# Optimization experiments

Hardware: AMD Instinct MI355X
Metric: run time of the kernel (lower is better)

## Reference

```python
import jax, jax.numpy as jnp
import numpy as np

B, N, DIM = 2, 8192, 3
K = 16            # num_neighbours (dilation=1)
R = 2048          # num_representitives
CIN, CL, COUT = 64, 16, 128
K2 = K * K


def _bn(x, g, b):
    # BatchNorm in eval mode with running_mean=0, running_var=1 -> affine
    return x * g + b


def setup_inputs() -> dict:
    key = jax.random.key(0)
    ks = jax.random.split(key, 24)
    r = lambda i, shape, s=1.0: jax.random.normal(ks[i], shape, jnp.float32) * s
    return {
        "points": r(0, (B, N, DIM)),
        "features": r(1, (B, N, CIN)),
        "lift_w": r(2, (CL, DIM), 0.3), "lift_b": r(3, (CL,), 0.1),
        "bn_lift_g": 1.0 + r(4, (CL,), 0.1), "bn_lift_b": r(5, (CL,), 0.1),
        "t1_w": r(6, (K2, DIM * K), 0.1), "t1_b": r(7, (K2,), 0.1),
        "bn1_g": 1.0 + r(8, (K2,), 0.1), "bn1_b": r(9, (K2,), 0.1),
        "t2_w": r(10, (K2, K2), 0.05), "t2_b": r(11, (K2,), 0.1),
        "bn2_g": 1.0 + r(12, (K2,), 0.1), "bn2_b": r(13, (K2,), 0.1),
        "t3_w": r(14, (K2, K2), 0.05), "t3_b": r(15, (K2,), 0.1),
        "bn3_g": 1.0 + r(16, (K2,), 0.1), "bn3_b": r(17, (K2,), 0.1),
        "conv_w": r(18, (COUT, CIN + CL, K), 0.05), "conv_b": r(19, (COUT,), 0.1),
        "rep_idx": jax.random.permutation(ks[20], N)[:R],
    }


def reference(points, features, lift_w, lift_b, bn_lift_g, bn_lift_b,
              t1_w, t1_b, bn1_g, bn1_b, t2_w, t2_b, bn2_g, bn2_b,
              t3_w, t3_b, bn3_g, bn3_b, conv_w, conv_b, rep_idx):
    b, n, _ = points.shape
    # ---- KNN (squared distance is order-equivalent to torch.cdist) ----
    sq = jnp.sum(points * points, -1)                                   # (b,n)
    d2 = sq[:, :, None] + sq[:, None, :] - 2.0 * jnp.einsum('bnd,bmd->bnm', points, points)
    _, idx = jax.lax.top_k(-d2, K + 1)                                  # (b,n,K+1)
    nn_idx = idx[:, :, 1:]                                              # drop self
    # ---- representative sampling + neighbor gather ----
    rep_pos = points[:, rep_idx]                                        # (b,R,3)
    nb_idx = nn_idx[:, rep_idx]                                         # (b,R,K)
    gather = jax.vmap(lambda arr, i: arr[i])
    nbr_pos = gather(points, nb_idx)                                    # (b,R,K,3)
    nbr_feat = gather(features, nb_idx)                                 # (b,R,K,CIN)
    # ---- X_conv ----
    p = (nbr_pos - rep_pos[:, :, None, :]).reshape(b * R, K, DIM)       # centered
    lifted = jax.nn.relu(_bn(p @ lift_w.T + lift_b, bn_lift_g, bn_lift_b))  # (bR,K,CL)
    feat = jnp.concatenate([lifted, nbr_feat.reshape(b * R, K, CIN)], -1)   # (bR,K,CL+CIN)
    pf = p.reshape(b * R, K * DIM)
    h = jax.nn.relu(_bn(pf @ t1_w.T + t1_b, bn1_g, bn1_b))
    h = jax.nn.relu(_bn(h @ t2_w.T + t2_b, bn2_g, bn2_b))
    T = _bn(h @ t3_w.T + t3_b, bn3_g, bn3_b).reshape(b * R, K, K)       # learned transform
    Tf = jnp.einsum('bij,bjc->bic', T, feat)                            # bmm, (bR,K,C)
    # Conv1d(C, COUT, kernel=K) over length K -> single output position
    out = jnp.einsum('bkc,ock->bo', Tf, conv_w) + conv_b                # (bR,COUT)
    return rep_pos, out.reshape(b, R, COUT)
```

## Files before the change

kernel.cpp:

```cpp
#include <hip/hip_runtime.h>
#include <float.h>

#define Bn 2
#define Nn 8192
#define Rr 2048
#define Kk 16
#define CIN 64
#define CL 16
#define COUT 128
#define K2c 256
#define GT (Bn*Rr)
#define FD (CL+CIN)
#define KC (Kk*FD)
#define MGB 8
#define SPLITK 4
#define CCAP 128

__global__ __launch_bounds__(256) void prep_kernel(
    const float* __restrict__ t1_w, const float* __restrict__ t2_w,
    const float* __restrict__ t3_w, const float* __restrict__ conv_w,
    const float* __restrict__ points,
    float* __restrict__ t1t, float* __restrict__ t2t,
    float* __restrict__ t3t, float* __restrict__ wp,
    float4* __restrict__ pts4)
{
  int i = blockIdx.x * 256 + threadIdx.x;
  if (i < K2c*48) { int j = i / 48, k = i - j*48; t1t[k*K2c + j] = t1_w[i]; }
  if (i < K2c*K2c) { int j = i >> 8, k = i & 255; t2t[k*K2c + j] = t2_w[i]; t3t[k*K2c + j] = t3_w[i]; }
  if (i < COUT*KC) {
    int o = i / KC, ck = i - o*KC;
    int c = ck >> 4, k = ck & 15;
    wp[(k*FD + c)*COUT + o] = conv_w[i];
  }
  if (i < Bn*Nn) {
    float x = points[i*3+0], y = points[i*3+1], z = points[i*3+2];
    float sq = __fadd_rn(__fadd_rn(__fmul_rn(x,x), __fmul_rn(y,y)), __fmul_rn(z,z));
    pts4[i] = make_float4(x, y, z, sq);
  }
}

__global__ __launch_bounds__(512, 4) void knn_kernel(
    const float4* __restrict__ pts4, const int* __restrict__ rep_idx,
    int* __restrict__ nb_idx, float* __restrict__ p_out,
    float* __restrict__ rep_pos_out)
{
  __shared__ float cbuf[8][512];
  __shared__ unsigned long long coll[8][CCAP];
  __shared__ float Lst[8][64];
  __shared__ float4 qS[8];
  __shared__ float  tauS[8];
  __shared__ int    ccnt[8];

  int t    = threadIdx.x;
  int lane = t & 63;
  int w    = t >> 6;
  int g0   = blockIdx.x * 8;
  int b    = g0 >> 11;
  const float4* pb4 = pts4 + (size_t)b*Nn;

  if (t < 8) {
    int g = g0 + t;
    int r = g & 2047;
    qS[t] = pb4[rep_idx[r]];
    ccnt[t] = 0;
  }
  __syncthreads();

  float qx[8], qy[8], qz[8], qw[8];
  #pragma unroll
  for (int q = 0; q < 8; q++) {
    float4 Q = qS[q];
    qx[q] = __uint_as_float(__builtin_amdgcn_readfirstlane(__float_as_uint(Q.x)));
    qy[q] = __uint_as_float(__builtin_amdgcn_readfirstlane(__float_as_uint(Q.y)));
    qz[q] = __uint_as_float(__builtin_amdgcn_readfirstlane(__float_as_uint(Q.z)));
    qw[q] = __uint_as_float(__builtin_amdgcn_readfirstlane(__float_as_uint(Q.w)));
  }

  float m[8];
  #pragma unroll
  for (int q = 0; q < 8; q++) m[q] = FLT_MAX;
  for (int i0 = 0; i0 < 16; i0 += 4) {
    float4 P0 = pb4[t + 512*(i0+0)];
    float4 P1 = pb4[t + 512*(i0+1)];
    float4 P2 = pb4[t + 512*(i0+2)];
    float4 P3 = pb4[t + 512*(i0+3)];
    #pragma unroll
    for (int q = 0; q < 8; q++) {
      float d0 = __fsub_rn(__fadd_rn(qw[q], P0.w), __fmul_rn(2.0f,
                 __fmaf_rn(qz[q], P0.z, __fmaf_rn(qy[q], P0.y, __fmul_rn(qx[q], P0.x)))));
      float d1 = __fsub_rn(__fadd_rn(qw[q], P1.w), __fmul_rn(2.0f,
                 __fmaf_rn(qz[q], P1.z, __fmaf_rn(qy[q], P1.y, __fmul_rn(qx[q], P1.x)))));
      float d2 = __fsub_rn(__fadd_rn(qw[q], P2.w), __fmul_rn(2.0f,
                 __fmaf_rn(qz[q], P2.z, __fmaf_rn(qy[q], P2.y, __fmul_rn(qx[q], P2.x)))));
      float d3 = __fsub_rn(__fadd_rn(qw[q], P3.w), __fmul_rn(2.0f,
                 __fmaf_rn(qz[q], P3.z, __fmaf_rn(qy[q], P3.y, __fmul_rn(qx[q], P3.x)))));
      m[q] = fminf(fminf(fminf(m[q], d0), fminf(d1, d2)), d3);
    }
  }

  #pragma unroll
  for (int q = 0; q < 8; q++) cbuf[q][t] = m[q];
  __syncthreads();

  {
    float C0 = FLT_MAX, C1 = FLT_MAX, C2 = FLT_MAX;
    #pragma unroll
    for (int j = 0; j < 8; j++) {
      float v = cbuf[w][lane + 64*j];
      float n2 = __builtin_amdgcn_fmed3f(C1, C2, v);
      float n1 = __builtin_amdgcn_fmed3f(C0, C1, v);
      float n0 = fminf(C0, v);
      C0 = n0; C1 = n1; C2 = n2;
    }
    Lst[w][lane] = C2;
  }
  __syncthreads();
  {
    float L = Lst[w][lane];
    int rk = 0;
    #pragma unroll 8
    for (int i = 0; i < 64; i++) {
      float Li = Lst[w][i];
      rk += (Li < L || (Li == L && i < lane)) ? 1 : 0;
    }
    if (rk == 5) tauS[w] = L;
  }
  __syncthreads();

  float tau[8];
  #pragma unroll
  for (int q = 0; q < 8; q++)
    tau[q] = __uint_as_float(__builtin_amdgcn_readfirstlane(__float_as_uint(tauS[q])));

  for (int i0 = 0; i0 < 16; i0 += 4) {
    float4 Pb[4];
    Pb[0] = pb4[t + 512*(i0+0)];
    Pb[1] = pb4[t + 512*(i0+1)];
    Pb[2] = pb4[t + 512*(i0+2)];
    Pb[3] = pb4[t + 512*(i0+3)];
    #pragma unroll
    for (int u = 0; u < 4; u++) {
      float4 P = Pb[u];
      int idx = t + 512*(i0+u);
      #pragma unroll
      for (int q = 0; q < 8; q++) {
        float dot = __fmaf_rn(qz[q], P.z, __fmaf_rn(qy[q], P.y, __fmul_rn(qx[q], P.x)));
        float d2  = __fsub_rn(__fadd_rn(qw[q], P.w), __fmul_rn(2.0f, dot));
        if (d2 <= tau[q]) {
          int pos = atomicAdd(&ccnt[q], 1);
          if (pos < CCAP) {
            unsigned f = __float_as_uint(d2);
            unsigned mono = f ^ ((unsigned)((int)f >> 31) | 0x80000000u);
            coll[q][pos] = ((unsigned long long)mono << 32) | (unsigned)idx;
          }
        }
      }
    }
  }
  __syncthreads();

  int cnt = __builtin_amdgcn_readfirstlane(ccnt[w]);
  if (cnt > CCAP) cnt = CCAP;
  unsigned long long k1 = (lane < cnt)      ? coll[w][lane]      : ~0ull;
  unsigned long long k2 = (lane + 64 < cnt) ? coll[w][lane + 64] : ~0ull;
  int r1 = 0, r2 = 0;
  for (int i = 0; i < cnt; i++) {
    unsigned long long ki = coll[w][i];
    r1 += (ki < k1) ? 1 : 0;
    r2 += (ki < k2) ? 1 : 0;
  }

  int g = g0 + w;
  float4 Q = qS[w];
  if (lane < cnt && r1 >= 1 && r1 <= 16) {
    int om = (int)(k1 & 0xFFFFFFFFull);
    nb_idx[g*Kk + r1 - 1] = om;
    float4 Pm = pb4[om];
    p_out[(g*Kk + r1 - 1)*3 + 0] = __fsub_rn(Pm.x, Q.x);
    p_out[(g*Kk + r1 - 1)*3 + 1] = __fsub_rn(Pm.y, Q.y);
    p_out[(g*Kk + r1 - 1)*3 + 2] = __fsub_rn(Pm.z, Q.z);
  }
  if (lane + 64 < cnt && r2 >= 1 && r2 <= 16) {
    int om = (int)(k2 & 0xFFFFFFFFull);
    nb_idx[g*Kk + r2 - 1] = om;
    float4 Pm = pb4[om];
    p_out[(g*Kk + r2 - 1)*3 + 0] = __fsub_rn(Pm.x, Q.x);
    p_out[(g*Kk + r2 - 1)*3 + 1] = __fsub_rn(Pm.y, Q.y);
    p_out[(g*Kk + r2 - 1)*3 + 2] = __fsub_rn(Pm.z, Q.z);
  }
  if (lane < 3) rep_pos_out[g*3 + lane] = (lane == 0 ? Q.x : (lane == 1 ? Q.y : Q.z));
}

__device__ __forceinline__ void fma_g(float4& a, float hv, const float4& wv) {
  a.x = fmaf(hv, wv.x, a.x);
  a.y = fmaf(hv, wv.y, a.y);
  a.z = fmaf(hv, wv.z, a.z);
  a.w = fmaf(hv, wv.w, a.w);
}

__global__ __launch_bounds__(512) void mlp_kernel(
    const float* __restrict__ p,
    const float* __restrict__ t1t, const float* __restrict__ t1_b,
    const float* __restrict__ g1v, const float* __restrict__ b1v,
    const float* __restrict__ t2t, const float* __restrict__ t2_b,
    const float* __restrict__ g2v, const float* __restrict__ b2v,
    const float* __restrict__ t3t, const float* __restrict__ t3_b,
    const float* __restrict__ g3v, const float* __restrict__ b3v,
    float* __restrict__ T_out)
{
  __shared__ float pf[48][MGB];
  __shared__ float hA[K2c][MGB];
  __shared__ float red[128*66];
  int t = threadIdx.x;
  int w = t >> 6, l = t & 63;
  int g0 = blockIdx.x * MGB;
  for (int e = t; e < MGB*48; e += 512) {
    int g = e / 48, k = e - g*48;
    pf[k][g] = p[(size_t)(g0+g)*48 + k];
  }
  __syncthreads();

  float4 acc[MGB];
  int col = t & 255;
  int h   = t >> 8;
  int cc  = col & 3, lr = col >> 2;

#define LDW(WSRC, K) (*(const float4*)&WSRC[(size_t)(K)*K2c + 4*l])

#define KSTAGE(WSRC, KDIM, HBUF, WB, KK, KNEXT)                        \
  {                                                                    \
    float4 wc = WB;                                                    \
    if ((KNEXT) < KDIM) WB = LDW(WSRC, KNEXT);                         \
    float4 ha = *(const float4*)&HBUF[KK][0];                          \
    float4 hb = *(const float4*)&HBUF[KK][4];                          \
    fma_g(acc[0], ha.x, wc); fma_g(acc[1], ha.y, wc);                  \
    fma_g(acc[2], ha.z, wc); fma_g(acc[3], ha.w, wc);                  \
    fma_g(acc[4], hb.x, wc); fma_g(acc[5], hb.y, wc);                  \
    fma_g(acc[6], hb.z, wc); fma_g(acc[7], hb.w, wc);                  \
  }

#define KLOOP(WSRC, KDIM, HBUF)                                        \
  {                                                                    \
    _Pragma("unroll")                                                  \
    for (int q = 0; q < MGB; q++) acc[q] = make_float4(0.f,0.f,0.f,0.f);\
    float4 wb0 = LDW(WSRC, w);                                         \
    float4 wb1 = (w + 8  < KDIM) ? LDW(WSRC, w + 8)  : wb0;            \
    float4 wb2 = (w + 16 < KDIM) ? LDW(WSRC, w + 16) : wb0;            \
    float4 wb3 = (w + 24 < KDIM) ? LDW(WSRC, w + 24) : wb0;            \
    for (int k = w; k < KDIM; k += 32) {                               \
      KSTAGE(WSRC, KDIM, HBUF, wb0, k,      k + 32)                    \
      if (k + 8  < KDIM) KSTAGE(WSRC, KDIM, HBUF, wb1, k + 8,  k + 40) \
      if (k + 16 < KDIM) KSTAGE(WSRC, KDIM, HBUF, wb2, k + 16, k + 48) \
      if (k + 24 < KDIM) KSTAGE(WSRC, KDIM, HBUF, wb3, k + 24, k + 56) \
    }                                                                  \
  }

#define WRITE_RED()                                                    \
  {                                                                    \
    if (w < 4) {                                                       \
      _Pragma("unroll")                                                \
      for (int q = 0; q < MGB; q++) {                                  \
        red[((w*4 + 0)*8 + q)*66 + l] = acc[q].x;                      \
        red[((w*4 + 1)*8 + q)*66 + l] = acc[q].y;                      \
        red[((w*4 + 2)*8 + q)*66 + l] = acc[q].z;                      \
        red[((w*4 + 3)*8 + q)*66 + l] = acc[q].w;                      \
      }                                                                \
    }                                                                  \
    __syncthreads();                                                   \
    if (w >= 4) {                                                      \
      int w2 = w - 4;                                                  \
      _Pragma("unroll")                                                \
      for (int q = 0; q < MGB; q++) {                                  \
        red[((w2*4 + 0)*8 + q)*66 + l] += acc[q].x;                    \
        red[((w2*4 + 1)*8 + q)*66 + l] += acc[q].y;                    \
        red[((w2*4 + 2)*8 + q)*66 + l] += acc[q].z;                    \
        red[((w2*4 + 3)*8 + q)*66 + l] += acc[q].w;                    \
      }                                                                \
    }                                                                  \
    __syncthreads();                                                   \
  }

#define REDUCE(S)                                                      \
  float S[4] = {0.f, 0.f, 0.f, 0.f};                                   \
  {                                                                    \
    _Pragma("unroll")                                                  \
    for (int ww = 0; ww < 4; ww++) {                                   \
      _Pragma("unroll")                                                \
      for (int qi = 0; qi < 4; qi++)                                   \
        S[qi] += red[((ww*4 + cc)*8 + (h*4 + qi))*66 + lr];            \
    }                                                                  \
  }

  KLOOP(t1t, 48, pf)
  WRITE_RED()
  {
    REDUCE(s)
    float bb = t1_b[col], gg = g1v[col], oo = b1v[col];
    float4 v;
    v.x = fmaxf(fmaf(s[0] + bb, gg, oo), 0.f);
    v.y = fmaxf(fmaf(s[1] + bb, gg, oo), 0.f);
    v.z = fmaxf(fmaf(s[2] + bb, gg, oo), 0.f);
    v.w = fmaxf(fmaf(s[3] + bb, gg, oo), 0.f);
    *(float4*)&hA[col][h*4] = v;
  }
  __syncthreads();

  KLOOP(t2t, K2c, hA)
  WRITE_RED()
  {
    REDUCE(s)
    float bb = t2_b[col], gg = g2v[col], oo = b2v[col];
    float4 v;
    v.x = fmaxf(fmaf(s[0] + bb, gg, oo), 0.f);
    v.y = fmaxf(fmaf(s[1] + bb, gg, oo), 0.f);
    v.z = fmaxf(fmaf(s[2] + bb, gg, oo), 0.f);
    v.w = fmaxf(fmaf(s[3] + bb, gg, oo), 0.f);
    *(float4*)&hA[col][h*4] = v;
  }
  __syncthreads();

  KLOOP(t3t, K2c, hA)
  WRITE_RED()
  {
    REDUCE(s)
    float bb = t3_b[col], gg = g3v[col], oo = b3v[col];
    #pragma unroll
    for (int qi = 0; qi < 4; qi++)
      T_out[(size_t)(g0 + h*4 + qi)*K2c + col] = fmaf(s[qi] + bb, gg, oo);
  }
#undef KLOOP
#undef KSTAGE
#undef LDW
#undef WRITE_RED
#undef REDUCE
}

__global__ __launch_bounds__(256) void tf_kernel(
    const float* __restrict__ T_in, const float* __restrict__ features,
    const float* __restrict__ p, const int* __restrict__ nb_idx,
    const float* __restrict__ lift_w, const float* __restrict__ lift_b,
    const float* __restrict__ bng, const float* __restrict__ bnb,
    float* __restrict__ Tf)
{
  __shared__ float T_s[4*K2c];
  __shared__ float f_s[4*KC];
  __shared__ float ps[4*48];
  __shared__ int   idxs[64];
  __shared__ float lw[48], lb2[16], lg[16], lo[16];
  int t = threadIdx.x;
  int g0 = blockIdx.x * 4;
  int b = g0 / Rr;
  for (int e = t; e < 4*K2c; e += 256) T_s[e] = T_in[(size_t)g0*K2c + e];
  if (t >= 32 && t < 224) {
    int e = t - 32;
    ps[e] = p[(size_t)g0*48 + e];
  }
  if (t < 64) idxs[t] = nb_idx[g0*16 + t];
  if (t >= 64 && t < 112)  lw[t-64]   = lift_w[t-64];
  if (t >= 112 && t < 128) lb2[t-112] = lift_b[t-112];
  if (t >= 224 && t < 240) lg[t-224]  = bng[t-224];
  if (t >= 240)            lo[t-240]  = bnb[t-240];
  __syncthreads();

  {
    int wv = t >> 6, ln = t & 63;
    for (int row = wv; row < 64; row += 4) {
      int gg = row >> 4, k = row & 15;
      f_s[gg*KC + k*FD + CL + ln] = features[((size_t)b*Nn + idxs[row])*CIN + ln];
    }
  }
  for (int e = t; e < 1024; e += 256) {
    int gg = e >> 8, rem = e & 255, k = rem >> 4, c = rem & 15;
    float acc = ps[gg*48 + k*3 + 0]*lw[c*3+0] + ps[gg*48 + k*3 + 1]*lw[c*3+1]
              + ps[gg*48 + k*3 + 2]*lw[c*3+2] + lb2[c];
    acc = acc*lg[c] + lo[c];
    f_s[gg*KC + k*FD + c] = fmaxf(acc, 0.f);
  }
  __syncthreads();

  int gg = t >> 6;
  int cl = t & 63;
  for (int ci = cl; ci < FD; ci += 64) {
    float fcol[16];
    #pragma unroll
    for (int j = 0; j < 16; j++) fcol[j] = f_s[gg*KC + j*FD + ci];
    #pragma unroll
    for (int k = 0; k < 16; k++) {
      float acc = 0.f;
      #pragma unroll
      for (int j = 0; j < 16; j++) acc = fmaf(T_s[gg*K2c + k*16 + j], fcol[j], acc);
      Tf[(size_t)(g0+gg)*KC + k*FD + ci] = acc;
    }
  }
}

__global__ __launch_bounds__(256) void gemm_kernel(
    const float* __restrict__ A,
    const float* __restrict__ Bm,
    float* __restrict__ part)
{
  __shared__ float As[16*36];
  __shared__ float Bs[16*COUT];
  int t = threadIdx.x;
  int m0 = blockIdx.x * 32;
  int ky = blockIdx.y;
  int kbase0 = ky * (KC/SPLITK);
  float acc[4][4];
  #pragma unroll
  for (int i = 0; i < 4; i++)
    #pragma unroll
    for (int j = 0; j < 4; j++) acc[i][j] = 0.f;
  int tn = t & 31, tm = t >> 5;

  for (int kt = 0; kt < KC/SPLITK; kt += 16) {
    int kb = kbase0 + kt;
    {
      int kcol = t & 15, row = t >> 4;
      As[kcol*36 + row]      = A[(size_t)(m0+row)*KC + kb + kcol];
      As[kcol*36 + row + 16] = A[(size_t)(m0+row+16)*KC + kb + kcol];
    }
    {
      int o = t & 127, kk2 = t >> 7;
      #pragma unroll
      for (int p4 = 0; p4 < 8; p4++) {
        int kk = kk2 + p4*2;
        Bs[kk*COUT + o] = Bm[(size_t)(kb+kk)*COUT + o];
      }
    }
    __syncthreads();
    #pragma unroll
    for (int kk = 0; kk < 16; kk++) {
      float4 a4 = *(const float4*)&As[kk*36 + tm*4];
      float4 b4 = *(const float4*)&Bs[kk*COUT + tn*4];
      float av[4] = {a4.x, a4.y, a4.z, a4.w};
      float bv[4] = {b4.x, b4.y, b4.z, b4.w};
      #pragma unroll
      for (int i = 0; i < 4; i++)
        #pragma unroll
        for (int j = 0; j < 4; j++) acc[i][j] = fmaf(av[i], bv[j], acc[i][j]);
    }
    __syncthreads();
  }
  #pragma unroll
  for (int i = 0; i < 4; i++) {
    float4 v = make_float4(acc[i][0], acc[i][1], acc[i][2], acc[i][3]);
    *(float4*)&part[((size_t)ky*GT + m0 + tm*4 + i)*COUT + tn*4] = v;
  }
}

__global__ __launch_bounds__(256) void reduce_kernel(
    const float* __restrict__ part, const float* __restrict__ conv_b,
    float* __restrict__ outp)
{
  int i = blockIdx.x*256 + threadIdx.x;
  float4 s = ((const float4*)conv_b)[i & 31];
  #pragma unroll
  for (int w = 0; w < SPLITK; w++) {
    float4 v = ((const float4*)(part + (size_t)w*GT*COUT))[i];
    s.x += v.x; s.y += v.y; s.z += v.z; s.w += v.w;
  }
  ((float4*)outp)[i] = s;
}

extern "C" void kernel_launch(void* const* d_in, const int* in_sizes, int n_in,
                              void* d_out, int out_size, void* d_ws, size_t ws_size,
                              hipStream_t stream) {
  const float* points   = (const float*)d_in[0];
  const float* features = (const float*)d_in[1];
  const float* lift_w   = (const float*)d_in[2];
  const float* lift_b   = (const float*)d_in[3];
  const float* bn_lift_g= (const float*)d_in[4];
  const float* bn_lift_b= (const float*)d_in[5];
  const float* t1_w     = (const float*)d_in[6];
  const float* t1_b     = (const float*)d_in[7];
  const float* bn1_g    = (const float*)d_in[8];
  const float* bn1_b    = (const float*)d_in[9];
  const float* t2_w     = (const float*)d_in[10];
  const float* t2_b     = (const float*)d_in[11];
  const float* bn2_g    = (const float*)d_in[12];
  const float* bn2_b    = (const float*)d_in[13];
  const float* t3_w     = (const float*)d_in[14];
  const float* t3_b     = (const float*)d_in[15];
  const float* bn3_g    = (const float*)d_in[16];
  const float* bn3_b    = (const float*)d_in[17];
  const float* conv_w   = (const float*)d_in[18];
  const float* conv_b   = (const float*)d_in[19];
  const int*   rep_idx  = (const int*)d_in[20];

  char* ws = (char*)d_ws;
  int*    nb   = (int*)   (ws + 0);
  float*  p    = (float*) (ws + 262144);
  float*  T    = (float*) (ws + 1048576);
  float*  Tf   = (float*) (ws + 5242880);
  float*  wp   = (float*) (ws + 26214400);
  float*  t1t  = (float*) (ws + 26869760);
  float*  t2t  = (float*) (ws + 26918912);
  float*  t3t  = (float*) (ws + 27181056);
  float*  part = (float*) (ws + 33554432);
  float4* pts4 = (float4*)(ws + 52428800);

  float* rep_pos = (float*)d_out;
  float* outp    = (float*)d_out + (size_t)GT*3;

  prep_kernel<<<640, 256, 0, stream>>>(t1_w, t2_w, t3_w, conv_w, points,
                                       t1t, t2t, t3t, wp, pts4);
  knn_kernel<<<GT/8, 512, 0, stream>>>(pts4, rep_idx, nb, p, rep_pos);
  mlp_kernel<<<GT/MGB, 512, 0, stream>>>(p, t1t, t1_b, bn1_g, bn1_b,
                                         t2t, t2_b, bn2_g, bn2_b,
                                         t3t, t3_b, bn3_g, bn3_b, T);
  tf_kernel<<<GT/4, 256, 0, stream>>>(T, features, p, nb,
                                      lift_w, lift_b, bn_lift_g, bn_lift_b, Tf);
  dim3 ggrid(GT/32, SPLITK);
  gemm_kernel<<<ggrid, 256, 0, stream>>>(Tf, wp, part);
  reduce_kernel<<<(GT*COUT/4)/256, 256, 0, stream>>>(part, conv_b, outp);
}
```

Before: 201.6 us.

## Fuse transform-bmm stage into MLP kernel to keep T in shared memory

Merges the per-representative transform application (T × features, including lift computation and neighbor feature gather) into the MLP kernel. T is written into the reused hA shared buffer instead of global memory, and the red buffer is reused for the feature tile, processed in two passes of four groups. This removes a global write and read of T and one kernel launch. In exchange, the bmm stage now runs with the MLP kernel's block count and shared memory footprint, which may lower parallelism for that phase.

```diff
diff --git a/kernel.cpp b/kernel.cpp
--- a/kernel.cpp
+++ b/kernel.cpp
@@ -198,7 +198,7 @@
   a.w = fmaf(hv, wv.w, a.w);
 }
 
-__global__ __launch_bounds__(512) void mlp_kernel(
+__global__ __launch_bounds__(512) void mlp_tf_kernel(
     const float* __restrict__ p,
     const float* __restrict__ t1t, const float* __restrict__ t1_b,
     const float* __restrict__ g1v, const float* __restrict__ b1v,
@@ -206,18 +206,29 @@
     const float* __restrict__ g2v, const float* __restrict__ b2v,
     const float* __restrict__ t3t, const float* __restrict__ t3_b,
     const float* __restrict__ g3v, const float* __restrict__ b3v,
-    float* __restrict__ T_out)
+    const float* __restrict__ features, const int* __restrict__ nb_idx,
+    const float* __restrict__ lift_w, const float* __restrict__ lift_b,
+    const float* __restrict__ bng, const float* __restrict__ bnb,
+    float* __restrict__ Tf)
 {
   __shared__ float pf[48][MGB];
   __shared__ float hA[K2c][MGB];
   __shared__ float red[128*66];
+  __shared__ int   idxs[128];
+  __shared__ float lw[48], lb2[16], lg[16], lo[16];
   int t = threadIdx.x;
   int w = t >> 6, l = t & 63;
   int g0 = blockIdx.x * MGB;
+  int bb_ = g0 / Rr;
   for (int e = t; e < MGB*48; e += 512) {
     int g = e / 48, k = e - g*48;
     pf[k][g] = p[(size_t)(g0+g)*48 + k];
   }
+  if (t < 128) idxs[t] = nb_idx[g0*16 + t];
+  else if (t >= 128 && t < 176) lw[t-128]  = lift_w[t-128];
+  else if (t >= 176 && t < 192) lb2[t-176] = lift_b[t-176];
+  else if (t >= 192 && t < 208) lg[t-192]  = bng[t-192];
+  else if (t >= 208 && t < 224) lo[t-208]  = bnb[t-208];
   __syncthreads();
 
   float4 acc[MGB];
@@ -321,77 +332,58 @@
 
   KLOOP(t3t, K2c, hA)
   WRITE_RED()
+  float* T_s = &hA[0][0];
   {
     REDUCE(s)
     float bb = t3_b[col], gg = g3v[col], oo = b3v[col];
     #pragma unroll
     for (int qi = 0; qi < 4; qi++)
-      T_out[(size_t)(g0 + h*4 + qi)*K2c + col] = fmaf(s[qi] + bb, gg, oo);
+      T_s[(h*4 + qi)*K2c + col] = fmaf(s[qi] + bb, gg, oo);
+  }
+  __syncthreads();
+
+  float* f_s = red;
+  for (int pass = 0; pass < 2; pass++) {
+    for (int row = w; row < 64; row += 8) {
+      int gg4 = row >> 4, k = row & 15;
+      int gl = pass*4 + gg4;
+      f_s[gg4*KC + k*FD + CL + l] =
+          features[((size_t)bb_*Nn + idxs[gl*16 + k])*CIN + l];
+    }
+    for (int e = t; e < 1024; e += 512) {
+      int gg4 = e >> 8, rem = e & 255, k = rem >> 4, c = rem & 15;
+      int gl = pass*4 + gg4;
+      float a = pf[k*3 + 0][gl]*lw[c*3+0] + pf[k*3 + 1][gl]*lw[c*3+1]
+              + pf[k*3 + 2][gl]*lw[c*3+2] + lb2[c];
+      a = a*lg[c] + lo[c];
+      f_s[gg4*KC + k*FD + c] = fmaxf(a, 0.f);
+    }
+    __syncthreads();
+    {
+      int gg4 = w >> 1, sub = w & 1;
+      int ci = sub*64 + l;
+      if (ci < FD) {
+        int gl = pass*4 + gg4;
+        float fcol[16];
+        #pragma unroll
+        for (int j = 0; j < 16; j++) fcol[j] = f_s[gg4*KC + j*FD + ci];
+        #pragma unroll
+        for (int k = 0; k < 16; k++) {
+          float a = 0.f;
+          #pragma unroll
+          for (int j = 0; j < 16; j++)
+            a = fmaf(T_s[gl*K2c + k*16 + j], fcol[j], a);
+          Tf[(size_t)(g0+gl)*KC + k*FD + ci] = a;
+        }
+      }
+    }
+    __syncthreads();
   }
 #undef KLOOP
 #undef KSTAGE
 #undef LDW
 #undef WRITE_RED
 #undef REDUCE
-}
-
-__global__ __launch_bounds__(256) void tf_kernel(
-    const float* __restrict__ T_in, const float* __restrict__ features,
-    const float* __restrict__ p, const int* __restrict__ nb_idx,
-    const float* __restrict__ lift_w, const float* __restrict__ lift_b,
-    const float* __restrict__ bng, const float* __restrict__ bnb,
-    float* __restrict__ Tf)
-{
-  __shared__ float T_s[4*K2c];
-  __shared__ float f_s[4*KC];
-  __shared__ float ps[4*48];
-  __shared__ int   idxs[64];
-  __shared__ float lw[48], lb2[16], lg[16], lo[16];
-  int t = threadIdx.x;
-  int g0 = blockIdx.x * 4;
-  int b = g0 / Rr;
-  for (int e = t; e < 4*K2c; e += 256) T_s[e] = T_in[(size_t)g0*K2c + e];
-  if (t >= 32 && t < 224) {
-    int e = t - 32;
-    ps[e] = p[(size_t)g0*48 + e];
-  }
-  if (t < 64) idxs[t] = nb_idx[g0*16 + t];
-  if (t >= 64 && t < 112)  lw[t-64]   = lift_w[t-64];
-  if (t >= 112 && t < 128) lb2[t-112] = lift_b[t-112];
-  if (t >= 224 && t < 240) lg[t-224]  = bng[t-224];
-  if (t >= 240)            lo[t-240]  = bnb[t-240];
-  __syncthreads();
-
-  {
-    int wv = t >> 6, ln = t & 63;
-    for (int row = wv; row < 64; row += 4) {
-      int gg = row >> 4, k = row & 15;
-      f_s[gg*KC + k*FD + CL + ln] = features[((size_t)b*Nn + idxs[row])*CIN + ln];
-    }
-  }
-  for (int e = t; e < 1024; e += 256) {
-    int gg = e >> 8, rem = e & 255, k = rem >> 4, c = rem & 15;
-    float acc = ps[gg*48 + k*3 + 0]*lw[c*3+0] + ps[gg*48 + k*3 + 1]*lw[c*3+1]
-              + ps[gg*48 + k*3 + 2]*lw[c*3+2] + lb2[c];
-    acc = acc*lg[c] + lo[c];
-    f_s[gg*KC + k*FD + c] = fmaxf(acc, 0.f);
-  }
-  __syncthreads();
-
-  int gg = t >> 6;
-  int cl = t & 63;
-  for (int ci = cl; ci < FD; ci += 64) {
-    float fcol[16];
-    #pragma unroll
-    for (int j = 0; j < 16; j++) fcol[j] = f_s[gg*KC + j*FD + ci];
-    #pragma unroll
-    for (int k = 0; k < 16; k++) {
-      float acc = 0.f;
-      #pragma unroll
-      for (int j = 0; j < 16; j++) acc = fmaf(T_s[gg*K2c + k*16 + j], fcol[j], acc);
-      Tf[(size_t)(g0+gg)*KC + k*FD + ci] = acc;
-    }
-  }
 }
 
 __global__ __launch_bounds__(256) void gemm_kernel(
@@ -490,7 +482,6 @@
   char* ws = (char*)d_ws;
   int*    nb   = (int*)   (ws + 0);
   float*  p    = (float*) (ws + 262144);
-  float*  T    = (float*) (ws + 1048576);
   float*  Tf   = (float*) (ws + 5242880);
   float*  wp   = (float*) (ws + 26214400);
   float*  t1t  = (float*) (ws + 26869760);
@@ -505,11 +496,12 @@
   prep_kernel<<<640, 256, 0, stream>>>(t1_w, t2_w, t3_w, conv_w, points,
                                        t1t, t2t, t3t, wp, pts4);
   knn_kernel<<<GT/8, 512, 0, stream>>>(pts4, rep_idx, nb, p, rep_pos);
-  mlp_kernel<<<GT/MGB, 512, 0, stream>>>(p, t1t, t1_b, bn1_g, bn1_b,
-                                         t2t, t2_b, bn2_g, bn2_b,
-                                         t3t, t3_b, bn3_g, bn3_b, T);
-  tf_kernel<<<GT/4, 256, 0, stream>>>(T, features, p, nb,
-                                      lift_w, lift_b, bn_lift_g, bn_lift_b, Tf);
+  mlp_tf_kernel<<<GT/MGB, 512, 0, stream>>>(p, t1t, t1_b, bn1_g, bn1_b,
+                                            t2t, t2_b, bn2_g, bn2_b,
+                                            t3t, t3_b, bn3_g, bn3_b,
+                                            features, nb,
+                                            lift_w, lift_b, bn_lift_g, bn_lift_b,
+                                            Tf);
   dim3 ggrid(GT/32, SPLITK);
   gemm_kernel<<<ggrid, 256, 0, stream>>>(Tf, wp, part);
   reduce_kernel<<<(GT*COUT/4)/256, 256, 0, stream>>>(part, conv_b, outp);
```

Measured after the change: 190.8 us (median of 3 runs). -5.4%, faster.
